# Optimization experiments

Measured on AMD Instinct MI355X. Metric: run time of the kernel, lower is better.

The kernel has to match this reference:

```python
import jax, jax.numpy as jnp
import numpy as np

EPS = 1e-8
DIGIT_TEMPERATURE = 1.0
SEED = 0
B, KMAX, V = 64, 16, 32000
DV, H = 10, 4096
# permute_prob table: prob_table[k] = permute_prob.get(k, 0.0)
_PROB = np.zeros(KMAX + 1, dtype=np.float32)
_PROB[2:] = 0.5
PROB_TABLE = jnp.asarray(_PROB)


def setup_inputs() -> dict:
    key = jax.random.key(0)
    ks = jax.random.split(key, 6)
    p_raw = jax.random.uniform(ks[0], (B, KMAX, V), dtype=jnp.float32)
    p_z = p_raw / p_raw.sum(axis=-1, keepdims=True)  # valid distributions per slot
    return {
        "p_z": p_z,
        "digit_logits_ref": jax.random.normal(ks[1], (B, DV), dtype=jnp.float32),
        "digit_logits_cf": jax.random.normal(ks[2], (B, DV), dtype=jnp.float32),
        "h_ans_ref": jax.random.normal(ks[3], (B, H), dtype=jnp.float32),
        "h_ans_cf": jax.random.normal(ks[4], (B, H), dtype=jnp.float32),
        "k_vals": jax.random.randint(ks[5], (B,), 0, KMAX + 1),
    }


def _js_divergence(p, q, eps=EPS):
    p = jnp.clip(p.astype(jnp.float32), eps)
    q = jnp.clip(q.astype(jnp.float32), eps)
    m = 0.5 * (p + q)
    log_m = jnp.log(m)
    kl_pm = (p * (jnp.log(p) - log_m)).sum(-1)
    kl_qm = (q * (jnp.log(q) - log_m)).sum(-1)
    return 0.5 * (kl_pm + kl_qm)


def _build_counterfactual_pz(p_z, k_vals):
    # Vectorized GS-mode counterfactual: per batch, with prob permute_prob[k]
    # (and k>1) permute the first k slots, otherwise temperature-warp them.
    bsz, kmax, vocab = p_z.shape
    key = jax.random.key(SEED)
    k_dec, k_perm, k_tau = jax.random.split(key, 3)
    u_dec = jax.random.uniform(k_dec, (bsz,))
    do_permute = (k_vals > 1) & (u_dec < PROB_TABLE[k_vals])  # [B]
    slots = jnp.arange(kmax)
    active = slots[None, :] < k_vals[:, None]  # [B, K]
    # ragged permutation of the first k slots: argsort random keys, inactive -> +inf
    u_perm = jax.random.uniform(k_perm, (bsz, kmax))
    perm = jnp.argsort(jnp.where(active, u_perm, jnp.inf), axis=1)  # stable: tail keeps order
    permuted = jnp.take_along_axis(p_z, perm[:, :, None], axis=1)
    # temperature warp: softmax(log(p)/tau), tau ~ U(0.7, 1.6) per slot
    tau = jax.random.uniform(k_tau, (bsz, kmax, 1), minval=0.7, maxval=1.6)
    warped = jax.nn.softmax(jnp.log(jnp.clip(p_z, EPS)) / tau, axis=-1)
    cf = jnp.where(do_permute[:, None, None], permuted, warped)
    return jnp.where(active[:, :, None], cf, p_z)


def reference(p_z, digit_logits_ref, digit_logits_cf, h_ans_ref, h_ans_cf, k_vals):
    p_cf_z = _build_counterfactual_pz(p_z, k_vals)
    # safe_softmax(logits, tau) == softmax(logits / tau)
    p_ref = jax.lax.stop_gradient(
        jax.nn.softmax(digit_logits_ref / DIGIT_TEMPERATURE, axis=-1))
    p_cf = jax.nn.softmax(digit_logits_cf / DIGIT_TEMPERATURE, axis=-1)
    js = _js_divergence(p_ref, p_cf).mean()
    loss_cf = jnp.log(jnp.float32(2.0)) - js
    ref_f = jax.lax.stop_gradient(h_ans_ref.astype(jnp.float32))
    cf_f = h_ans_cf.astype(jnp.float32)
    ref_norm = ref_f / jnp.clip(jnp.linalg.norm(ref_f, axis=-1, keepdims=True), 1e-12)
    cf_norm = cf_f / jnp.clip(jnp.linalg.norm(cf_f, axis=-1, keepdims=True), 1e-12)
    cos_sim = (ref_norm * cf_norm).sum(-1).mean()
    loss_dep = cos_sim - 1.0  # cf_mode == 'gs'
    dep_norm = jnp.linalg.norm(ref_f - cf_f, axis=-1).mean()
    return loss_cf, loss_dep, dep_norm, p_cf_z
```

## Files before the change

### kernel.cpp

```cpp
#include <hip/hip_runtime.h>
#include <stdint.h>

#define NB    64
#define KMAX  16
#define VV    32000
#define DVV   10
#define HH    4096
#define NROWS (NB*KMAX)
#define EPSF  1e-8f
#define NQ    8000

typedef float floatx4 __attribute__((ext_vector_type(4)));

__device__ __forceinline__ uint32_t rotl32(uint32_t v, int r) { return (v << r) | (v >> (32 - r)); }

__device__ __forceinline__ void tf2x32(uint32_t k0, uint32_t k1, uint32_t c0, uint32_t c1,
                                       uint32_t& o0, uint32_t& o1) {
    uint32_t ks2 = k0 ^ k1 ^ 0x1BD11BDAu;
    uint32_t x0 = c0 + k0, x1 = c1 + k1;
    const int RA[4] = {13, 15, 26, 6};
    const int RB[4] = {17, 29, 16, 24};
#pragma unroll
    for (int i = 0; i < 4; ++i) { x0 += x1; x1 = rotl32(x1, RA[i]); x1 ^= x0; }
    x0 += k1; x1 += ks2 + 1u;
#pragma unroll
    for (int i = 0; i < 4; ++i) { x0 += x1; x1 = rotl32(x1, RB[i]); x1 ^= x0; }
    x0 += ks2; x1 += k0 + 2u;
#pragma unroll
    for (int i = 0; i < 4; ++i) { x0 += x1; x1 = rotl32(x1, RA[i]); x1 ^= x0; }
    x0 += k0; x1 += k1 + 3u;
#pragma unroll
    for (int i = 0; i < 4; ++i) { x0 += x1; x1 = rotl32(x1, RB[i]); x1 ^= x0; }
    x0 += k1; x1 += ks2 + 4u;
#pragma unroll
    for (int i = 0; i < 4; ++i) { x0 += x1; x1 = rotl32(x1, RA[i]); x1 ^= x0; }
    x0 += ks2; x1 += k0 + 5u;
    o0 = x0; o1 = x1;
}

__device__ __forceinline__ float bits_to_u01(uint32_t bits) {
    uint32_t fb = (bits >> 9) | 0x3F800000u;
    return __uint_as_float(fb) - 1.0f;
}

__device__ __forceinline__ void nt_store4(float* p, float a, float b, float c, float d) {
    floatx4 v = {a, b, c, d};
    __builtin_nontemporal_store(v, (floatx4*)p);
}

__global__ __launch_bounds__(1024) void setup_kernel(const int* __restrict__ k_vals,
                                                     int* __restrict__ src_arr,
                                                     float* __restrict__ itau_arr) {
    const int j = threadIdx.x;
    const int b = j >> 4, s = j & 15;

    __shared__ float su[NROWS];
    __shared__ int   sk[NB];
    __shared__ int   sdp[NB];

    uint32_t a0, b0, a1, b1, a2, b2;
    tf2x32(0u, 0u, 0u, 3u, a0, b0);
    tf2x32(0u, 0u, 1u, 4u, a1, b1);
    tf2x32(0u, 0u, 2u, 5u, a2, b2);
    const uint32_t kdec0 = a0, kdec1 = a1;
    const uint32_t kperm0 = a2, kperm1 = b0;
    const uint32_t ktau0 = b1, ktau1 = b2;

    uint32_t y0, y1, pb, tb;
    if (j < 512) { tf2x32(kperm0, kperm1, (uint32_t)j, (uint32_t)(j + 512), y0, y1); pb = y0; }
    else         { tf2x32(kperm0, kperm1, (uint32_t)(j - 512), (uint32_t)j, y0, y1); pb = y1; }
    su[j] = bits_to_u01(pb);
    if (j < 512) { tf2x32(ktau0, ktau1, (uint32_t)j, (uint32_t)(j + 512), y0, y1); tb = y0; }
    else         { tf2x32(ktau0, ktau1, (uint32_t)(j - 512), (uint32_t)j, y0, y1); tb = y1; }
    float tau = fmaxf(0.7f, bits_to_u01(tb) * 0.9f + 0.7f);
    float itau = 1.0f / tau;

    if (j < NB) {
        uint32_t bits;
        if (j < 32) { tf2x32(kdec0, kdec1, (uint32_t)j, (uint32_t)(j + 32), y0, y1); bits = y0; }
        else        { tf2x32(kdec0, kdec1, (uint32_t)(j - 32), (uint32_t)j, y0, y1); bits = y1; }
        float u_dec = bits_to_u01(bits);
        int k = k_vals[j];
        float prob = (k >= 2) ? 0.5f : 0.0f;
        sk[j] = k;
        sdp[j] = (k > 1) && (u_dec < prob);
    }
    __syncthreads();

    const int k = sk[b];
    const bool dp = sdp[b] != 0;
    const float INF = __int_as_float(0x7F800000);
    const float myk = (s < k) ? su[j] : INF;

    int r = 0;
#pragma unroll
    for (int t = 0; t < KMAX; ++t) {
        float kt = (t < k) ? su[(b << 4) + t] : INF;
        r += (kt < myk) || (kt == myk && t < s);
    }

    if (s >= k)      { src_arr[j] = s;            itau_arr[j] = 0.0f; }
    else if (dp)     { src_arr[(b << 4) + r] = s; itau_arr[(b << 4) + r] = 0.0f; }
    else             { src_arr[j] = -1;           itau_arr[j] = itau; }
}

__global__ __launch_bounds__(256) void rowred_kernel(const float* __restrict__ hr,
                                                     const float* __restrict__ hc,
                                                     float* __restrict__ cosb,
                                                     float* __restrict__ depb) {
    int b = blockIdx.x;
    const float4* r4 = (const float4*)(hr + (size_t)b * HH);
    const float4* c4 = (const float4*)(hc + (size_t)b * HH);
    float srr = 0.f, scc = 0.f, sxc = 0.f, sdd = 0.f;
    for (int i = threadIdx.x; i < HH / 4; i += 256) {
        float4 r = r4[i], c = c4[i];
        srr += r.x * r.x + r.y * r.y + r.z * r.z + r.w * r.w;
        scc += c.x * c.x + c.y * c.y + c.z * c.z + c.w * c.w;
        sxc += r.x * c.x + r.y * c.y + r.z * c.z + r.w * c.w;
        float dx = r.x - c.x, dy = r.y - c.y, dz = r.z - c.z, dw = r.w - c.w;
        sdd += dx * dx + dy * dy + dz * dz + dw * dw;
    }
#pragma unroll
    for (int o = 32; o; o >>= 1) {
        srr += __shfl_down(srr, o, 64);
        scc += __shfl_down(scc, o, 64);
        sxc += __shfl_down(sxc, o, 64);
        sdd += __shfl_down(sdd, o, 64);
    }
    __shared__ float red[4][4];
    int w = threadIdx.x >> 6;
    if ((threadIdx.x & 63) == 0) { red[w][0] = srr; red[w][1] = scc; red[w][2] = sxc; red[w][3] = sdd; }
    __syncthreads();
    if (threadIdx.x == 0) {
        float t0 = 0.f, t1 = 0.f, t2 = 0.f, t3 = 0.f;
        for (int i = 0; i < 4; ++i) { t0 += red[i][0]; t1 += red[i][1]; t2 += red[i][2]; t3 += red[i][3]; }
        float nr = fmaxf(sqrtf(t0), 1e-12f);
        float nc = fmaxf(sqrtf(t1), 1e-12f);
        cosb[b] = t2 / (nr * nc);
        depb[b] = sqrtf(t3);
    }
}

__global__ void finalize_kernel(const float* __restrict__ dlr, const float* __restrict__ dlc,
                                const float* __restrict__ cosb, const float* __restrict__ depb,
                                float* __restrict__ out) {
    int b = threadIdx.x;
    float lr[DVV], lc[DVV];
    float mr = -1e30f, mc = -1e30f;
#pragma unroll
    for (int v = 0; v < DVV; ++v) {
        lr[v] = dlr[b * DVV + v]; lc[v] = dlc[b * DVV + v];
        mr = fmaxf(mr, lr[v]); mc = fmaxf(mc, lc[v]);
    }
    float sr = 0.f, sc = 0.f;
#pragma unroll
    for (int v = 0; v < DVV; ++v) {
        lr[v] = expf(lr[v] - mr); sr += lr[v];
        lc[v] = expf(lc[v] - mc); sc += lc[v];
    }
    float js = 0.f;
#pragma unroll
    for (int v = 0; v < DVV; ++v) {
        float p = fmaxf(lr[v] / sr, EPSF);
        float q = fmaxf(lc[v] / sc, EPSF);
        float m = 0.5f * (p + q);
        float lm = logf(m);
        js += 0.5f * (p * (logf(p) - lm) + q * (logf(q) - lm));
    }
    float cs = cosb[b], dp = depb[b];
#pragma unroll
    for (int o = 32; o; o >>= 1) {
        js += __shfl_down(js, o, 64);
        cs += __shfl_down(cs, o, 64);
        dp += __shfl_down(dp, o, 64);
    }
    if (b == 0) {
        out[0] = logf(2.0f) - js * (1.0f / 64.0f);
        out[1] = cs * (1.0f / 64.0f) - 1.0f;
        out[2] = dp * (1.0f / 64.0f);
    }
}

__global__ __launch_bounds__(1024) void cf_main_kernel(const float* __restrict__ p_z,
                                                       const int* __restrict__ src_arr,
                                                       const float* __restrict__ itau_arr,
                                                       float* __restrict__ out) {
    const int row = blockIdx.x;
    const int b = row >> 4;
    const int src = src_arr[row];
    const int tid = threadIdx.x;
    float* dst = out + (size_t)row * VV;

    if (src >= 0) {
        const float* s = p_z + ((size_t)((b << 4) + src)) * VV;
#pragma unroll
        for (int i = 0; i < 8; ++i) {
            const int q = tid + (i << 10);
            if (q < NQ - 1) {
                float4 v = *(const float4*)(s + (q << 2) + 1);
                nt_store4(dst + (q << 2) + 1, v.x, v.y, v.z, v.w);
            }
        }
        if (tid == 0) dst[0] = s[0];
        if (tid == 1) {
            dst[VV - 3] = s[VV - 3];
            dst[VV - 2] = s[VV - 2];
            dst[VV - 1] = s[VV - 1];
        }
        return;
    }

    const float it = itau_arr[row];
    const float* s = p_z + (size_t)row * VV;
    float4 r[8];
    float e0 = 0.f, t0 = 0.f, t1 = 0.f, t2 = 0.f;
    float lsum = 0.f;
#pragma unroll
    for (int i = 0; i < 8; ++i) {
        const int q = tid + (i << 10);
        if (q < NQ - 1) {
            float4 v = *(const float4*)(s + (q << 2) + 1);
            v.x = exp2f(__log2f(fmaxf(v.x, EPSF)) * it);
            v.y = exp2f(__log2f(fmaxf(v.y, EPSF)) * it);
            v.z = exp2f(__log2f(fmaxf(v.z, EPSF)) * it);
            v.w = exp2f(__log2f(fmaxf(v.w, EPSF)) * it);
            r[i] = v;
            lsum += v.x + v.y + v.z + v.w;
        } else {
            r[i] = make_float4(0.f, 0.f, 0.f, 0.f);
        }
    }
    if (tid == 0) { e0 = exp2f(__log2f(fmaxf(s[0], EPSF)) * it); lsum += e0; }
    if (tid == 1) {
        t0 = exp2f(__log2f(fmaxf(s[VV - 3], EPSF)) * it);
        t1 = exp2f(__log2f(fmaxf(s[VV - 2], EPSF)) * it);
        t2 = exp2f(__log2f(fmaxf(s[VV - 1], EPSF)) * it);
        lsum += t0 + t1 + t2;
    }
    __shared__ float red[16];
    float t = lsum;
#pragma unroll
    for (int o = 32; o; o >>= 1) t += __shfl_down(t, o, 64);
    if ((tid & 63) == 0) red[tid >> 6] = t;
    __syncthreads();
    if (tid < 64) {
        float u = (tid < 16) ? red[tid] : 0.0f;
#pragma unroll
        for (int o = 8; o; o >>= 1) u += __shfl_down(u, o, 64);
        if (tid == 0) red[0] = u;
    }
    __syncthreads();
    const float scale = 1.0f / red[0];

#pragma unroll
    for (int i = 0; i < 8; ++i) {
        const int q = tid + (i << 10);
        if (q < NQ - 1) {
            nt_store4(dst + (q << 2) + 1,
                      r[i].x * scale, r[i].y * scale, r[i].z * scale, r[i].w * scale);
        }
    }
    if (tid == 0) dst[0] = e0 * scale;
    if (tid == 1) {
        dst[VV - 3] = t0 * scale;
        dst[VV - 2] = t1 * scale;
        dst[VV - 1] = t2 * scale;
    }
}

extern "C" void kernel_launch(void* const* d_in, const int* in_sizes, int n_in,
                              void* d_out, int out_size, void* d_ws, size_t ws_size,
                              hipStream_t stream) {
    const float* p_z = (const float*)d_in[0];
    const float* dlr = (const float*)d_in[1];
    const float* dlc = (const float*)d_in[2];
    const float* hr  = (const float*)d_in[3];
    const float* hc  = (const float*)d_in[4];
    const int*   kv  = (const int*)d_in[5];
    float* out = (float*)d_out;

    int*   src_arr  = (int*)d_ws;
    float* itau_arr = (float*)d_ws + NROWS;
    float* cosb     = (float*)d_ws + 2 * NROWS;
    float* depb     = cosb + NB;

    setup_kernel<<<1, 1024, 0, stream>>>(kv, src_arr, itau_arr);
    cf_main_kernel<<<NROWS, 1024, 0, stream>>>(p_z, src_arr, itau_arr, out + 3);
    rowred_kernel<<<NB, 256, 0, stream>>>(hr, hc, cosb, depb);
    finalize_kernel<<<1, 64, 0, stream>>>(dlr, dlc, cosb, depb, out);
}
```

Measured before the change: 57.53 us.

## Fuse RNG/permutation setup into main kernel and use regular stores

Removes the separate single-block setup kernel. Each row block now recomputes its source slot and inverse temperature with 16 lanes, using a shuffle-based rank computation, so one launch and its serialization point go away. Nontemporal stores are also replaced with ordinary float4 stores. The cost is redundant Threefry work in every block before the streaming phase begins, and the stores may now pollute the cache.

```diff
diff --git a/kernel.cpp b/kernel.cpp
--- a/kernel.cpp
+++ b/kernel.cpp
@@ -10,8 +10,6 @@
 #define EPSF  1e-8f
 #define NQ    8000
 
-typedef float floatx4 __attribute__((ext_vector_type(4)));
-
 __device__ __forceinline__ uint32_t rotl32(uint32_t v, int r) { return (v << r) | (v >> (32 - r)); }
 
 __device__ __forceinline__ void tf2x32(uint32_t k0, uint32_t k1, uint32_t c0, uint32_t c1,
@@ -43,65 +41,142 @@
     return __uint_as_float(fb) - 1.0f;
 }
 
-__device__ __forceinline__ void nt_store4(float* p, float a, float b, float c, float d) {
-    floatx4 v = {a, b, c, d};
-    __builtin_nontemporal_store(v, (floatx4*)p);
-}
-
-__global__ __launch_bounds__(1024) void setup_kernel(const int* __restrict__ k_vals,
-                                                     int* __restrict__ src_arr,
-                                                     float* __restrict__ itau_arr) {
-    const int j = threadIdx.x;
-    const int b = j >> 4, s = j & 15;
-
-    __shared__ float su[NROWS];
-    __shared__ int   sk[NB];
-    __shared__ int   sdp[NB];
-
-    uint32_t a0, b0, a1, b1, a2, b2;
-    tf2x32(0u, 0u, 0u, 3u, a0, b0);
-    tf2x32(0u, 0u, 1u, 4u, a1, b1);
-    tf2x32(0u, 0u, 2u, 5u, a2, b2);
-    const uint32_t kdec0 = a0, kdec1 = a1;
-    const uint32_t kperm0 = a2, kperm1 = b0;
-    const uint32_t ktau0 = b1, ktau1 = b2;
-
-    uint32_t y0, y1, pb, tb;
-    if (j < 512) { tf2x32(kperm0, kperm1, (uint32_t)j, (uint32_t)(j + 512), y0, y1); pb = y0; }
-    else         { tf2x32(kperm0, kperm1, (uint32_t)(j - 512), (uint32_t)j, y0, y1); pb = y1; }
-    su[j] = bits_to_u01(pb);
-    if (j < 512) { tf2x32(ktau0, ktau1, (uint32_t)j, (uint32_t)(j + 512), y0, y1); tb = y0; }
-    else         { tf2x32(ktau0, ktau1, (uint32_t)(j - 512), (uint32_t)j, y0, y1); tb = y1; }
-    float tau = fmaxf(0.7f, bits_to_u01(tb) * 0.9f + 0.7f);
-    float itau = 1.0f / tau;
-
-    if (j < NB) {
+__global__ __launch_bounds__(1024) void cf_main_kernel(const float* __restrict__ p_z,
+                                                       const int* __restrict__ k_vals,
+                                                       float* __restrict__ out) {
+    const int row = blockIdx.x;
+    const int b = row >> 4, s = row & 15;
+    const int tid = threadIdx.x;
+    float* dst = out + (size_t)row * VV;
+
+    __shared__ int   s_src;
+    __shared__ float s_itau;
+
+    if (tid < 16) {
+        const int t = tid;
+        uint32_t a0, b0_, a1, b1_, a2, b2_, y0, y1;
+        tf2x32(0u, 0u, 0u, 3u, a0, b0_);
+        tf2x32(0u, 0u, 1u, 4u, a1, b1_);
+        tf2x32(0u, 0u, 2u, 5u, a2, b2_);
+        const uint32_t kdec0 = a0, kdec1 = a1;
+        const uint32_t kperm0 = a2, kperm1 = b0_;
+        const uint32_t ktau0 = b1_, ktau1 = b2_;
+
+        const int k = k_vals[b];
+
         uint32_t bits;
-        if (j < 32) { tf2x32(kdec0, kdec1, (uint32_t)j, (uint32_t)(j + 32), y0, y1); bits = y0; }
-        else        { tf2x32(kdec0, kdec1, (uint32_t)(j - 32), (uint32_t)j, y0, y1); bits = y1; }
-        float u_dec = bits_to_u01(bits);
-        int k = k_vals[j];
-        float prob = (k >= 2) ? 0.5f : 0.0f;
-        sk[j] = k;
-        sdp[j] = (k > 1) && (u_dec < prob);
-    }
-    __syncthreads();
-
-    const int k = sk[b];
-    const bool dp = sdp[b] != 0;
-    const float INF = __int_as_float(0x7F800000);
-    const float myk = (s < k) ? su[j] : INF;
-
-    int r = 0;
-#pragma unroll
-    for (int t = 0; t < KMAX; ++t) {
-        float kt = (t < k) ? su[(b << 4) + t] : INF;
-        r += (kt < myk) || (kt == myk && t < s);
-    }
-
-    if (s >= k)      { src_arr[j] = s;            itau_arr[j] = 0.0f; }
-    else if (dp)     { src_arr[(b << 4) + r] = s; itau_arr[(b << 4) + r] = 0.0f; }
-    else             { src_arr[j] = -1;           itau_arr[j] = itau; }
+        if (b < 32) { tf2x32(kdec0, kdec1, (uint32_t)b, (uint32_t)(b + 32), y0, y1); bits = y0; }
+        else        { tf2x32(kdec0, kdec1, (uint32_t)(b - 32), (uint32_t)b, y0, y1); bits = y1; }
+        const float u_dec = bits_to_u01(bits);
+        const bool dp = (k > 1) && (u_dec < ((k >= 2) ? 0.5f : 0.0f));
+
+        const int j = (b << 4) + t;
+        uint32_t pb;
+        if (j < 512) { tf2x32(kperm0, kperm1, (uint32_t)j, (uint32_t)(j + 512), y0, y1); pb = y0; }
+        else         { tf2x32(kperm0, kperm1, (uint32_t)(j - 512), (uint32_t)j, y0, y1); pb = y1; }
+        const float up = bits_to_u01(pb);
+
+        const float INF = __int_as_float(0x7F800000);
+        const float keyt = (t < k) ? up : INF;
+        int r = 0;
+#pragma unroll
+        for (int tt = 0; tt < KMAX; ++tt) {
+            float kt = __shfl(keyt, tt, 64);
+            r += (kt < keyt) || (kt == keyt && tt < t);
+        }
+
+        if (s >= k)  { if (t == 0) { s_src = s; s_itau = 0.f; } }
+        else if (dp) { if (r == s) { s_src = t; s_itau = 0.f; } }
+        else if (t == 0) {
+            const int js = (b << 4) + s;
+            uint32_t tb;
+            if (js < 512) { tf2x32(ktau0, ktau1, (uint32_t)js, (uint32_t)(js + 512), y0, y1); tb = y0; }
+            else          { tf2x32(ktau0, ktau1, (uint32_t)(js - 512), (uint32_t)js, y0, y1); tb = y1; }
+            const float tau = fmaxf(0.7f, bits_to_u01(tb) * 0.9f + 0.7f);
+            s_src = -1; s_itau = 1.0f / tau;
+        }
+    }
+    __syncthreads();
+
+    const int src = s_src;
+
+    if (src >= 0) {
+        const float* sp = p_z + ((size_t)((b << 4) + src)) * VV;
+#pragma unroll
+        for (int i = 0; i < 8; ++i) {
+            const int q = tid + (i << 10);
+            if (q < NQ - 1) {
+                float4 v = *(const float4*)(sp + (q << 2) + 1);
+                *(float4*)(dst + (q << 2) + 1) = v;
+            }
+        }
+        if (tid == 0) dst[0] = sp[0];
+        if (tid == 1) {
+            dst[VV - 3] = sp[VV - 3];
+            dst[VV - 2] = sp[VV - 2];
+            dst[VV - 1] = sp[VV - 1];
+        }
+        return;
+    }
+
+    const float it = s_itau;
+    const float* sp = p_z + (size_t)row * VV;
+    float4 r[8];
+    float e0 = 0.f, t0 = 0.f, t1 = 0.f, t2 = 0.f;
+    float lsum = 0.f;
+#pragma unroll
+    for (int i = 0; i < 8; ++i) {
+        const int q = tid + (i << 10);
+        if (q < NQ - 1) {
+            float4 v = *(const float4*)(sp + (q << 2) + 1);
+            v.x = exp2f(__log2f(fmaxf(v.x, EPSF)) * it);
+            v.y = exp2f(__log2f(fmaxf(v.y, EPSF)) * it);
+            v.z = exp2f(__log2f(fmaxf(v.z, EPSF)) * it);
+            v.w = exp2f(__log2f(fmaxf(v.w, EPSF)) * it);
+            r[i] = v;
+            lsum += v.x + v.y + v.z + v.w;
+        } else {
+            r[i] = make_float4(0.f, 0.f, 0.f, 0.f);
+        }
+    }
+    if (tid == 0) { e0 = exp2f(__log2f(fmaxf(sp[0], EPSF)) * it); lsum += e0; }
+    if (tid == 1) {
+        t0 = exp2f(__log2f(fmaxf(sp[VV - 3], EPSF)) * it);
+        t1 = exp2f(__log2f(fmaxf(sp[VV - 2], EPSF)) * it);
+        t2 = exp2f(__log2f(fmaxf(sp[VV - 1], EPSF)) * it);
+        lsum += t0 + t1 + t2;
+    }
+    __shared__ float red[16];
+    float t = lsum;
+#pragma unroll
+    for (int o = 32; o; o >>= 1) t += __shfl_down(t, o, 64);
+    if ((tid & 63) == 0) red[tid >> 6] = t;
+    __syncthreads();
+    if (tid < 64) {
+        float u = (tid < 16) ? red[tid] : 0.0f;
+#pragma unroll
+        for (int o = 8; o; o >>= 1) u += __shfl_down(u, o, 64);
+        if (tid == 0) red[0] = u;
+    }
+    __syncthreads();
+    const float scale = 1.0f / red[0];
+
+#pragma unroll
+    for (int i = 0; i < 8; ++i) {
+        const int q = tid + (i << 10);
+        if (q < NQ - 1) {
+            float4 st;
+            st.x = r[i].x * scale; st.y = r[i].y * scale;
+            st.z = r[i].z * scale; st.w = r[i].w * scale;
+            *(float4*)(dst + (q << 2) + 1) = st;
+        }
+    }
+    if (tid == 0) dst[0] = e0 * scale;
+    if (tid == 1) {
+        dst[VV - 3] = t0 * scale;
+        dst[VV - 2] = t1 * scale;
+        dst[VV - 1] = t2 * scale;
+    }
 }
 
 __global__ __launch_bounds__(256) void rowred_kernel(const float* __restrict__ hr,
@@ -181,93 +256,6 @@
     }
 }
 
-__global__ __launch_bounds__(1024) void cf_main_kernel(const float* __restrict__ p_z,
-                                                       const int* __restrict__ src_arr,
-                                                       const float* __restrict__ itau_arr,
-                                                       float* __restrict__ out) {
-    const int row = blockIdx.x;
-    const int b = row >> 4;
-    const int src = src_arr[row];
-    const int tid = threadIdx.x;
-    float* dst = out + (size_t)row * VV;
-
-    if (src >= 0) {
-        const float* s = p_z + ((size_t)((b << 4) + src)) * VV;
-#pragma unroll
-        for (int i = 0; i < 8; ++i) {
-            const int q = tid + (i << 10);
-            if (q < NQ - 1) {
-                float4 v = *(const float4*)(s + (q << 2) + 1);
-                nt_store4(dst + (q << 2) + 1, v.x, v.y, v.z, v.w);
-            }
-        }
-        if (tid == 0) dst[0] = s[0];
-        if (tid == 1) {
-            dst[VV - 3] = s[VV - 3];
-            dst[VV - 2] = s[VV - 2];
-            dst[VV - 1] = s[VV - 1];
-        }
-        return;
-    }
-
-    const float it = itau_arr[row];
-    const float* s = p_z + (size_t)row * VV;
-    float4 r[8];
-    float e0 = 0.f, t0 = 0.f, t1 = 0.f, t2 = 0.f;
-    float lsum = 0.f;
-#pragma unroll
-    for (int i = 0; i < 8; ++i) {
-        const int q = tid + (i << 10);
-        if (q < NQ - 1) {
-            float4 v = *(const float4*)(s + (q << 2) + 1);
-            v.x = exp2f(__log2f(fmaxf(v.x, EPSF)) * it);
-            v.y = exp2f(__log2f(fmaxf(v.y, EPSF)) * it);
-            v.z = exp2f(__log2f(fmaxf(v.z, EPSF)) * it);
-            v.w = exp2f(__log2f(fmaxf(v.w, EPSF)) * it);
-            r[i] = v;
-            lsum += v.x + v.y + v.z + v.w;
-        } else {
-            r[i] = make_float4(0.f, 0.f, 0.f, 0.f);
-        }
-    }
-    if (tid == 0) { e0 = exp2f(__log2f(fmaxf(s[0], EPSF)) * it); lsum += e0; }
-    if (tid == 1) {
-        t0 = exp2f(__log2f(fmaxf(s[VV - 3], EPSF)) * it);
-        t1 = exp2f(__log2f(fmaxf(s[VV - 2], EPSF)) * it);
-        t2 = exp2f(__log2f(fmaxf(s[VV - 1], EPSF)) * it);
-        lsum += t0 + t1 + t2;
-    }
-    __shared__ float red[16];
-    float t = lsum;
-#pragma unroll
-    for (int o = 32; o; o >>= 1) t += __shfl_down(t, o, 64);
-    if ((tid & 63) == 0) red[tid >> 6] = t;
-    __syncthreads();
-    if (tid < 64) {
-        float u = (tid < 16) ? red[tid] : 0.0f;
-#pragma unroll
-        for (int o = 8; o; o >>= 1) u += __shfl_down(u, o, 64);
-        if (tid == 0) red[0] = u;
-    }
-    __syncthreads();
-    const float scale = 1.0f / red[0];
-
-#pragma unroll
-    for (int i = 0; i < 8; ++i) {
-        const int q = tid + (i << 10);
-        if (q < NQ - 1) {
-            nt_store4(dst + (q << 2) + 1,
-                      r[i].x * scale, r[i].y * scale, r[i].z * scale, r[i].w * scale);
-        }
-    }
-    if (tid == 0) dst[0] = e0 * scale;
-    if (tid == 1) {
-        dst[VV - 3] = t0 * scale;
-        dst[VV - 2] = t1 * scale;
-        dst[VV - 1] = t2 * scale;
-    }
-}
-
 extern "C" void kernel_launch(void* const* d_in, const int* in_sizes, int n_in,
                               void* d_out, int out_size, void* d_ws, size_t ws_size,
                               hipStream_t stream) {
@@ -279,13 +267,10 @@
     const int*   kv  = (const int*)d_in[5];
     float* out = (float*)d_out;
 
-    int*   src_arr  = (int*)d_ws;
-    float* itau_arr = (float*)d_ws + NROWS;
-    float* cosb     = (float*)d_ws + 2 * NROWS;
-    float* depb     = cosb + NB;
-
-    setup_kernel<<<1, 1024, 0, stream>>>(kv, src_arr, itau_arr);
-    cf_main_kernel<<<NROWS, 1024, 0, stream>>>(p_z, src_arr, itau_arr, out + 3);
+    float* cosb = (float*)d_ws;
+    float* depb = cosb + NB;
+
+    cf_main_kernel<<<NROWS, 1024, 0, stream>>>(p_z, kv, out + 3);
     rowred_kernel<<<NB, 256, 0, stream>>>(hr, hc, cosb, depb);
     finalize_kernel<<<1, 64, 0, stream>>>(dlr, dlc, cosb, depb, out);
 }
```

After: 57.97 us. About the same (+0.8%).

## Schedule warp rows first via rowmap, halve block size, drop nontemporal stores

Applied to the files above, without the earlier changes.

The setup kernel now builds a row map that puts the temperature-warped rows, which carry the transcendental work, ahead of the copy rows, so the main kernel dispatches the heavy blocks first and load balance improves. The main kernel drops from 1024 to 512 threads per block, with each thread handling 16 float4s instead of 8. Nontemporal stores are replaced with ordinary stores. The risks are higher register pressure from 16 float4s held per thread, and possible loss of the cache-bypass benefit on the large output write.

```diff
diff --git a/kernel.cpp b/kernel.cpp
--- a/kernel.cpp
+++ b/kernel.cpp
@@ -10,8 +10,6 @@
 #define EPSF  1e-8f
 #define NQ    8000
 
-typedef float floatx4 __attribute__((ext_vector_type(4)));
-
 __device__ __forceinline__ uint32_t rotl32(uint32_t v, int r) { return (v << r) | (v >> (32 - r)); }
 
 __device__ __forceinline__ void tf2x32(uint32_t k0, uint32_t k1, uint32_t c0, uint32_t c1,
@@ -43,20 +41,18 @@
     return __uint_as_float(fb) - 1.0f;
 }
 
-__device__ __forceinline__ void nt_store4(float* p, float a, float b, float c, float d) {
-    floatx4 v = {a, b, c, d};
-    __builtin_nontemporal_store(v, (floatx4*)p);
-}
-
 __global__ __launch_bounds__(1024) void setup_kernel(const int* __restrict__ k_vals,
                                                      int* __restrict__ src_arr,
-                                                     float* __restrict__ itau_arr) {
+                                                     float* __restrict__ itau_arr,
+                                                     int* __restrict__ rowmap) {
     const int j = threadIdx.x;
     const int b = j >> 4, s = j & 15;
 
     __shared__ float su[NROWS];
     __shared__ int   sk[NB];
     __shared__ int   sdp[NB];
+    __shared__ int   wcnt[16];
+    __shared__ int   woff[17];
 
     uint32_t a0, b0, a1, b1, a2, b2;
     tf2x32(0u, 0u, 0u, 3u, a0, b0);
@@ -102,6 +98,112 @@
     if (s >= k)      { src_arr[j] = s;            itau_arr[j] = 0.0f; }
     else if (dp)     { src_arr[(b << 4) + r] = s; itau_arr[(b << 4) + r] = 0.0f; }
     else             { src_arr[j] = -1;           itau_arr[j] = itau; }
+
+    const bool iswarp = (s < k) && !dp;
+    const uint64_t mask = __ballot(iswarp);
+    const int lane = j & 63, w = j >> 6;
+    const int lanePre = __popcll(mask & ((lane == 0) ? 0ull : (~0ull >> (64 - lane))));
+    if (lane == 0) wcnt[w] = __popcll(mask);
+    __syncthreads();
+    if (j == 0) {
+        woff[0] = 0;
+        for (int i = 0; i < 16; ++i) woff[i + 1] = woff[i] + wcnt[i];
+    }
+    __syncthreads();
+    const int nwarp = woff[16];
+    const int wpre = woff[w] + lanePre;
+    const int pos = iswarp ? wpre : nwarp + (j - wpre);
+    rowmap[pos] = j;
+}
+
+__global__ __launch_bounds__(512) void cf_main_kernel(const float* __restrict__ p_z,
+                                                      const int* __restrict__ src_arr,
+                                                      const float* __restrict__ itau_arr,
+                                                      const int* __restrict__ rowmap,
+                                                      float* __restrict__ out) {
+    const int row = rowmap[blockIdx.x];
+    const int b = row >> 4;
+    const int src = src_arr[row];
+    const int tid = threadIdx.x;
+    float* dst = out + (size_t)row * VV;
+
+    if (src >= 0) {
+        const float* sp = p_z + ((size_t)((b << 4) + src)) * VV;
+#pragma unroll
+        for (int i = 0; i < 16; ++i) {
+            const int q = tid + (i << 9);
+            if (q < NQ - 1) {
+                float4 v = *(const float4*)(sp + (q << 2) + 1);
+                *(float4*)(dst + (q << 2) + 1) = v;
+            }
+        }
+        if (tid == 0) dst[0] = sp[0];
+        if (tid == 1) {
+            dst[VV - 3] = sp[VV - 3];
+            dst[VV - 2] = sp[VV - 2];
+            dst[VV - 1] = sp[VV - 1];
+        }
+        return;
+    }
+
+    const float it = itau_arr[row];
+    const float* sp = p_z + (size_t)row * VV;
+    float4 r[16];
+    float e0 = 0.f, t0 = 0.f, t1 = 0.f, t2 = 0.f;
+    float lsum = 0.f;
+#pragma unroll
+    for (int i = 0; i < 16; ++i) {
+        const int q = tid + (i << 9);
+        if (q < NQ - 1) {
+            float4 v = *(const float4*)(sp + (q << 2) + 1);
+            v.x = exp2f(__log2f(fmaxf(v.x, EPSF)) * it);
+            v.y = exp2f(__log2f(fmaxf(v.y, EPSF)) * it);
+            v.z = exp2f(__log2f(fmaxf(v.z, EPSF)) * it);
+            v.w = exp2f(__log2f(fmaxf(v.w, EPSF)) * it);
+            r[i] = v;
+            lsum += v.x + v.y + v.z + v.w;
+        } else {
+            r[i] = make_float4(0.f, 0.f, 0.f, 0.f);
+        }
+    }
+    if (tid == 0) { e0 = exp2f(__log2f(fmaxf(sp[0], EPSF)) * it); lsum += e0; }
+    if (tid == 1) {
+        t0 = exp2f(__log2f(fmaxf(sp[VV - 3], EPSF)) * it);
+        t1 = exp2f(__log2f(fmaxf(sp[VV - 2], EPSF)) * it);
+        t2 = exp2f(__log2f(fmaxf(sp[VV - 1], EPSF)) * it);
+        lsum += t0 + t1 + t2;
+    }
+    __shared__ float red[8];
+    float t = lsum;
+#pragma unroll
+    for (int o = 32; o; o >>= 1) t += __shfl_down(t, o, 64);
+    if ((tid & 63) == 0) red[tid >> 6] = t;
+    __syncthreads();
+    if (tid < 64) {
+        float u = (tid < 8) ? red[tid] : 0.0f;
+#pragma unroll
+        for (int o = 4; o; o >>= 1) u += __shfl_down(u, o, 64);
+        if (tid == 0) red[0] = u;
+    }
+    __syncthreads();
+    const float scale = 1.0f / red[0];
+
+#pragma unroll
+    for (int i = 0; i < 16; ++i) {
+        const int q = tid + (i << 9);
+        if (q < NQ - 1) {
+            float4 st;
+            st.x = r[i].x * scale; st.y = r[i].y * scale;
+            st.z = r[i].z * scale; st.w = r[i].w * scale;
+            *(float4*)(dst + (q << 2) + 1) = st;
+        }
+    }
+    if (tid == 0) dst[0] = e0 * scale;
+    if (tid == 1) {
+        dst[VV - 3] = t0 * scale;
+        dst[VV - 2] = t1 * scale;
+        dst[VV - 1] = t2 * scale;
+    }
 }
 
 __global__ __launch_bounds__(256) void rowred_kernel(const float* __restrict__ hr,
@@ -181,93 +283,6 @@
     }
 }
 
-__global__ __launch_bounds__(1024) void cf_main_kernel(const float* __restrict__ p_z,
-                                                       const int* __restrict__ src_arr,
-                                                       const float* __restrict__ itau_arr,
-                                                       float* __restrict__ out) {
-    const int row = blockIdx.x;
-    const int b = row >> 4;
-    const int src = src_arr[row];
-    const int tid = threadIdx.x;
-    float* dst = out + (size_t)row * VV;
-
-    if (src >= 0) {
-        const float* s = p_z + ((size_t)((b << 4) + src)) * VV;
-#pragma unroll
-        for (int i = 0; i < 8; ++i) {
-            const int q = tid + (i << 10);
-            if (q < NQ - 1) {
-                float4 v = *(const float4*)(s + (q << 2) + 1);
-                nt_store4(dst + (q << 2) + 1, v.x, v.y, v.z, v.w);
-            }
-        }
-        if (tid == 0) dst[0] = s[0];
-        if (tid == 1) {
-            dst[VV - 3] = s[VV - 3];
-            dst[VV - 2] = s[VV - 2];
-            dst[VV - 1] = s[VV - 1];
-        }
-        return;
-    }
-
-    const float it = itau_arr[row];
-    const float* s = p_z + (size_t)row * VV;
-    float4 r[8];
-    float e0 = 0.f, t0 = 0.f, t1 = 0.f, t2 = 0.f;
-    float lsum = 0.f;
-#pragma unroll
-    for (int i = 0; i < 8; ++i) {
-        const int q = tid + (i << 10);
-        if (q < NQ - 1) {
-            float4 v = *(const float4*)(s + (q << 2) + 1);
-            v.x = exp2f(__log2f(fmaxf(v.x, EPSF)) * it);
-            v.y = exp2f(__log2f(fmaxf(v.y, EPSF)) * it);
-            v.z = exp2f(__log2f(fmaxf(v.z, EPSF)) * it);
-            v.w = exp2f(__log2f(fmaxf(v.w, EPSF)) * it);
-            r[i] = v;
-            lsum += v.x + v.y + v.z + v.w;
-        } else {
-            r[i] = make_float4(0.f, 0.f, 0.f, 0.f);
-        }
-    }
-    if (tid == 0) { e0 = exp2f(__log2f(fmaxf(s[0], EPSF)) * it); lsum += e0; }
-    if (tid == 1) {
-        t0 = exp2f(__log2f(fmaxf(s[VV - 3], EPSF)) * it);
-        t1 = exp2f(__log2f(fmaxf(s[VV - 2], EPSF)) * it);
-        t2 = exp2f(__log2f(fmaxf(s[VV - 1], EPSF)) * it);
-        lsum += t0 + t1 + t2;
-    }
-    __shared__ float red[16];
-    float t = lsum;
-#pragma unroll
-    for (int o = 32; o; o >>= 1) t += __shfl_down(t, o, 64);
-    if ((tid & 63) == 0) red[tid >> 6] = t;
-    __syncthreads();
-    if (tid < 64) {
-        float u = (tid < 16) ? red[tid] : 0.0f;
-#pragma unroll
-        for (int o = 8; o; o >>= 1) u += __shfl_down(u, o, 64);
-        if (tid == 0) red[0] = u;
-    }
-    __syncthreads();
-    const float scale = 1.0f / red[0];
-
-#pragma unroll
-    for (int i = 0; i < 8; ++i) {
-        const int q = tid + (i << 10);
-        if (q < NQ - 1) {
-            nt_store4(dst + (q << 2) + 1,
-                      r[i].x * scale, r[i].y * scale, r[i].z * scale, r[i].w * scale);
-        }
-    }
-    if (tid == 0) dst[0] = e0 * scale;
-    if (tid == 1) {
-        dst[VV - 3] = t0 * scale;
-        dst[VV - 2] = t1 * scale;
-        dst[VV - 1] = t2 * scale;
-    }
-}
-
 extern "C" void kernel_launch(void* const* d_in, const int* in_sizes, int n_in,
                               void* d_out, int out_size, void* d_ws, size_t ws_size,
                               hipStream_t stream) {
@@ -281,11 +296,12 @@
 
     int*   src_arr  = (int*)d_ws;
     float* itau_arr = (float*)d_ws + NROWS;
-    float* cosb     = (float*)d_ws + 2 * NROWS;
+    int*   rowmap   = (int*)d_ws + 2 * NROWS;
+    float* cosb     = (float*)d_ws + 3 * NROWS;
     float* depb     = cosb + NB;
 
-    setup_kernel<<<1, 1024, 0, stream>>>(kv, src_arr, itau_arr);
-    cf_main_kernel<<<NROWS, 1024, 0, stream>>>(p_z, src_arr, itau_arr, out + 3);
+    setup_kernel<<<1, 1024, 0, stream>>>(kv, src_arr, itau_arr, rowmap);
+    cf_main_kernel<<<NROWS, 512, 0, stream>>>(p_z, src_arr, itau_arr, rowmap, out + 3);
     rowred_kernel<<<NB, 256, 0, stream>>>(hr, hc, cosb, depb);
     finalize_kernel<<<1, 64, 0, stream>>>(dlr, dlc, cosb, depb, out);
 }
```

Result: slower. 61.37 us (+6.7%).
